# Kernel tuning notes

Hardware: AMD Instinct MI355X
Metric: run time of the kernel (lower is better)

The kernel has to match this reference:

```python
import jax, jax.numpy as jnp
import numpy as np

N = 524288          # events per batch
NUM_NODES = 1_000_000
D = 64              # memory_dim


def gru_cell(x, h, W_ih, W_hh, b_ih, b_hh):
    # torch.nn.GRUCell math; gates ordered (r, z, n)
    gi = x @ W_ih.T + b_ih          # [N, 3D]
    gh = h @ W_hh.T + b_hh          # [N, 3D]
    i_r, i_z, i_n = jnp.split(gi, 3, axis=-1)
    h_r, h_z, h_n = jnp.split(gh, 3, axis=-1)
    r = jax.nn.sigmoid(i_r + h_r)
    z = jax.nn.sigmoid(i_z + h_z)
    n = jnp.tanh(i_n + r * h_n)
    return (1.0 - z) * n + z * h


def setup_inputs() -> dict:
    key = jax.random.key(0)
    ks = jax.random.split(key, 9)
    scale = 1.0 / np.sqrt(D).astype(np.float32)
    return {
        "node_ids": jax.random.randint(ks[0], (N,), 0, NUM_NODES, dtype=jnp.int64)
        if jax.config.jax_enable_x64 else jax.random.randint(ks[0], (N,), 0, NUM_NODES, dtype=jnp.int32),
        "node_embeddings": jax.random.normal(ks[1], (N, D), jnp.float32),
        "timestamps": jax.random.uniform(ks[2], (N,), jnp.float32) * 1000.0,
        "node_memory": jax.random.normal(ks[3], (NUM_NODES, D), jnp.float32) * 0.1,
        "last_update_time": jax.random.uniform(ks[4], (NUM_NODES,), jnp.float32) * 500.0,
        "W_time": jax.random.normal(ks[5], (1, D), jnp.float32) * 0.1,
        "b_time": jnp.zeros((D,), jnp.float32),
        "W_ih": jax.random.normal(ks[6], (3 * D, D), jnp.float32) * scale,
        "W_hh": jax.random.normal(ks[7], (3 * D, D), jnp.float32) * scale,
        "b_ih": jnp.zeros((3 * D,), jnp.float32),
        "b_hh": jnp.zeros((3 * D,), jnp.float32),
    }


def reference(node_ids, node_embeddings, timestamps, node_memory, last_update_time,
              W_time, b_time, W_ih, W_hh, b_ih, b_hh):
    # gather persistent state
    current_memory = node_memory[node_ids]                          # [N, D]
    time_deltas = timestamps - last_update_time[node_ids]           # [N]
    # nn.Linear(1, D): out = dt * W_time[0] + b_time
    time_encoding = time_deltas[:, None] * W_time[0] + b_time       # [N, D]
    updated_memory = gru_cell(node_embeddings + time_encoding, current_memory,
                              W_ih, W_hh, b_ih, b_hh)               # [N, D]
    # scatter write-back (detached in torch)
    new_node_memory = node_memory.at[node_ids].set(jax.lax.stop_gradient(updated_memory))
    new_last_update_time = last_update_time.at[node_ids].set(jax.lax.stop_gradient(timestamps))
    return updated_memory, new_node_memory, new_last_update_time
```

## Files before the change

kernel.cpp:

```cpp
#include <hip/hip_runtime.h>
#include <cstdint>
#include <cstddef>

#define DD 64

typedef float    f32x4  __attribute__((ext_vector_type(4)));
typedef _Float16 f16x8  __attribute__((ext_vector_type(8)));
typedef _Float16 f16x4  __attribute__((ext_vector_type(4)));

__device__ __forceinline__ float sigmoidf_(float x) {
    return 1.0f / (1.0f + __expf(-x));
}
__device__ __forceinline__ float tanh_fast(float x) {
    float ax = fabsf(x);
    float t = 1.0f - 2.0f / (1.0f + __expf(2.0f * ax));
    return copysignf(t, x);
}
__device__ __forceinline__ f32x4 MFMA(f32x4 c, f16x8 a, f16x8 b) {
    return __builtin_amdgcn_mfma_f32_16x16x32_f16(a, b, c, 0, 0, 0);
}

__global__ void k_init(int* __restrict__ winner, int num_nodes) {
    int i = blockIdx.x * blockDim.x + threadIdx.x;
    if (i < num_nodes) winner[i] = -1;
}
__global__ void k_vote(const int* __restrict__ ids, int* __restrict__ winner, int n) {
    int i = blockIdx.x * blockDim.x + threadIdx.x;
    if (i < n) atomicMax(&winner[ids[i]], i);
}

__global__ void k_prep(const float* __restrict__ Wih, const float* __restrict__ Whh,
                       _Float16* __restrict__ bhi, _Float16* __restrict__ blo)
{
    int f = blockIdx.x;
    int l = threadIdx.x;
    int g = f >> 2, s = f & 3;
    int c = g * 16 + (l & 15);
    int grp = c >> 6, d = c & 63;
    int kbase = s * 32 + (l >> 4) * 8;
    int row = (grp == 0) ? d : (grp == 1) ? 64 + d : 128 + d;

    f16x8 hv, lv;
    for (int j = 0; j < 8; ++j) {
        int k = kbase + j;
        float v;
        if (grp <= 1)      v = (k < 64) ? Wih[row * 64 + k] : Whh[row * 64 + (k - 64)];
        else if (grp == 2) v = (k < 64) ? Wih[row * 64 + k] : 0.0f;
        else               v = (k < 64) ? 0.0f : Whh[row * 64 + (k - 64)];
        _Float16 h = (_Float16)v;
        hv[j] = h;
        lv[j] = (_Float16)(v - (float)h);
    }
    size_t off = ((size_t)f * 64 + l);
    ((f16x8*)bhi)[off] = hv;
    ((f16x8*)blo)[off] = lv;
}

__global__ __launch_bounds__(256, 3) void k_gru(
    const int* __restrict__ ids,
    const float* __restrict__ emb,
    const float* __restrict__ ts,
    const float* __restrict__ mem,
    const float* __restrict__ lut,
    const float* __restrict__ Wt,
    const float* __restrict__ bt,
    const float* __restrict__ bih,
    const float* __restrict__ bhh,
    const _Float16* __restrict__ bhi,
    const _Float16* __restrict__ blo,
    const int* __restrict__ winner,
    float* __restrict__ out0,
    float* __restrict__ out1,
    int n)
{
    __shared__ _Float16 xhh[64][136];
    __shared__ _Float16 xhl[64][72];
    __shared__ int sid[64];
    __shared__ int swin[64];

    const int w    = threadIdx.x >> 6;
    const int l    = threadIdx.x & 63;
    const int col  = l & 15;
    const int rowg = l >> 4;
    const int d    = w * 16 + col;

    const long base = (long)blockIdx.x * 64;
    const bool full = (base + 64 <= (long)n);

    const int  e16 = w * 16 + col;
    const long evA = base + e16;
    int idA = 0, winA = 0; float dtA = 0.f;
    if (full || evA < n) {
        idA  = ids[evA];
        dtA  = ts[evA] - lut[idA];
        winA = (winner[idA] == (int)evA) ? 1 : 0;
    }
    if (l < 16) { sid[e16] = idA; swin[e16] = winA; }

    f32x4 xv0, xv1, xv2, xv3, hv0, hv1, hv2, hv3;
    float dt0, dt1, dt2, dt3;
    {
        int   i0 = __shfl(idA, 0 * 4 + rowg), i1 = __shfl(idA, 1 * 4 + rowg);
        int   i2 = __shfl(idA, 2 * 4 + rowg), i3 = __shfl(idA, 3 * 4 + rowg);
        dt0 = __shfl(dtA, 0 * 4 + rowg); dt1 = __shfl(dtA, 1 * 4 + rowg);
        dt2 = __shfl(dtA, 2 * 4 + rowg); dt3 = __shfl(dtA, 3 * 4 + rowg);
        const f32x4* emb4 = (const f32x4*)emb;
        const f32x4* mem4 = (const f32x4*)mem;
        const size_t e0 = (size_t)(base + w * 16 + 0 * 4 + rowg) * 16 + col;
        const size_t e1 = (size_t)(base + w * 16 + 1 * 4 + rowg) * 16 + col;
        const size_t e2 = (size_t)(base + w * 16 + 2 * 4 + rowg) * 16 + col;
        const size_t e3 = (size_t)(base + w * 16 + 3 * 4 + rowg) * 16 + col;
        if (full) {
            xv0 = __builtin_nontemporal_load(&emb4[e0]);
            xv1 = __builtin_nontemporal_load(&emb4[e1]);
            xv2 = __builtin_nontemporal_load(&emb4[e2]);
            xv3 = __builtin_nontemporal_load(&emb4[e3]);
            hv0 = mem4[(size_t)i0 * 16 + col];
            hv1 = mem4[(size_t)i1 * 16 + col];
            hv2 = mem4[(size_t)i2 * 16 + col];
            hv3 = mem4[(size_t)i3 * 16 + col];
        } else {
            f32x4 z = {0.f, 0.f, 0.f, 0.f};
            xv0 = xv1 = xv2 = xv3 = hv0 = hv1 = hv2 = hv3 = z;
            if (base + w * 16 + 0 * 4 + rowg < n) { xv0 = emb4[e0]; hv0 = mem4[(size_t)i0 * 16 + col]; }
            if (base + w * 16 + 1 * 4 + rowg < n) { xv1 = emb4[e1]; hv1 = mem4[(size_t)i1 * 16 + col]; }
            if (base + w * 16 + 2 * 4 + rowg < n) { xv2 = emb4[e2]; hv2 = mem4[(size_t)i2 * 16 + col]; }
            if (base + w * 16 + 3 * 4 + rowg < n) { xv3 = emb4[e3]; hv3 = mem4[(size_t)i3 * 16 + col]; }
        }
    }

    const f32x4 wt4 = ((const f32x4*)Wt)[col];
    const f32x4 bt4 = ((const f32x4*)bt)[col];
    {
        #define CONV_WRITE(XV, HV, DT, IT)                                           \
        {                                                                            \
            int r = w * 16 + (IT) * 4 + rowg;                                        \
            f32x4 x = XV;                                                            \
            x.x = fmaf(DT, wt4.x, x.x + bt4.x);                                      \
            x.y = fmaf(DT, wt4.y, x.y + bt4.y);                                      \
            x.z = fmaf(DT, wt4.z, x.z + bt4.z);                                      \
            x.w = fmaf(DT, wt4.w, x.w + bt4.w);                                      \
            f16x4 xh, xl, hh;                                                        \
            _Float16 a;                                                              \
            a = (_Float16)x.x; xh[0] = a; xl[0] = (_Float16)(x.x - (float)a);        \
            a = (_Float16)x.y; xh[1] = a; xl[1] = (_Float16)(x.y - (float)a);        \
            a = (_Float16)x.z; xh[2] = a; xl[2] = (_Float16)(x.z - (float)a);        \
            a = (_Float16)x.w; xh[3] = a; xl[3] = (_Float16)(x.w - (float)a);        \
            hh[0] = (_Float16)(HV).x; hh[1] = (_Float16)(HV).y;                      \
            hh[2] = (_Float16)(HV).z; hh[3] = (_Float16)(HV).w;                      \
            *(f16x4*)&xhh[r][col * 4]      = xh;                                     \
            *(f16x4*)&xhl[r][col * 4]      = xl;                                     \
            *(f16x4*)&xhh[r][64 + col * 4] = hh;                                     \
        }
        CONV_WRITE(xv0, hv0, dt0, 0)
        CONV_WRITE(xv1, hv1, dt1, 1)
        CONV_WRITE(xv2, hv2, dt2, 2)
        CONV_WRITE(xv3, hv3, dt3, 3)
        #undef CONV_WRITE
    }

    const f16x8* H = (const f16x8*)bhi;
    const f16x8* L = (const f16x8*)blo;
    f16x8 BRh0 = H[(size_t)(w * 4 + 0) * 64 + l];
    f16x8 BRh1 = H[(size_t)(w * 4 + 1) * 64 + l];
    f16x8 BRh2 = H[(size_t)(w * 4 + 2) * 64 + l];
    f16x8 BRh3 = H[(size_t)(w * 4 + 3) * 64 + l];
    f16x8 BRl0 = L[(size_t)(w * 4 + 0) * 64 + l];
    f16x8 BRl1 = L[(size_t)(w * 4 + 1) * 64 + l];
    f16x8 BZh0 = H[(size_t)((4 + w) * 4 + 0) * 64 + l];
    f16x8 BZh1 = H[(size_t)((4 + w) * 4 + 1) * 64 + l];
    f16x8 BZh2 = H[(size_t)((4 + w) * 4 + 2) * 64 + l];
    f16x8 BZh3 = H[(size_t)((4 + w) * 4 + 3) * 64 + l];
    f16x8 BZl0 = L[(size_t)((4 + w) * 4 + 0) * 64 + l];
    f16x8 BZl1 = L[(size_t)((4 + w) * 4 + 1) * 64 + l];
    f16x8 BIh0 = H[(size_t)((8 + w) * 4 + 0) * 64 + l];
    f16x8 BIh1 = H[(size_t)((8 + w) * 4 + 1) * 64 + l];
    f16x8 BIl0 = L[(size_t)((8 + w) * 4 + 0) * 64 + l];
    f16x8 BIl1 = L[(size_t)((8 + w) * 4 + 1) * 64 + l];
    f16x8 BHh0 = H[(size_t)((12 + w) * 4 + 2) * 64 + l];
    f16x8 BHh1 = H[(size_t)((12 + w) * 4 + 3) * 64 + l];

    const float bR  = bih[d] + bhh[d];
    const float bZ  = bih[64 + d] + bhh[64 + d];
    const float bIN = bih[128 + d];
    const float bHN = bhh[128 + d];

    __syncthreads();

    #pragma unroll
    for (int mt = 0; mt < 4; ++mt) {
        const int arow = mt * 16 + col;
        const int k0   = rowg * 8;
        f16x8 Ah0 = *(const f16x8*)&xhh[arow][0 * 32 + k0];
        f16x8 Ah1 = *(const f16x8*)&xhh[arow][1 * 32 + k0];
        f16x8 Ah2 = *(const f16x8*)&xhh[arow][2 * 32 + k0];
        f16x8 Ah3 = *(const f16x8*)&xhh[arow][3 * 32 + k0];
        f16x8 Al0 = *(const f16x8*)&xhl[arow][0 * 32 + k0];
        f16x8 Al1 = *(const f16x8*)&xhl[arow][1 * 32 + k0];

        f32x4 aR = {0,0,0,0}, aZ = {0,0,0,0}, aI = {0,0,0,0}, aH = {0,0,0,0};
        __builtin_amdgcn_s_setprio(1);
        aR = MFMA(aR, Ah0, BRh0); aR = MFMA(aR, Ah0, BRl0); aR = MFMA(aR, Al0, BRh0);
        aR = MFMA(aR, Ah1, BRh1); aR = MFMA(aR, Ah1, BRl1); aR = MFMA(aR, Al1, BRh1);
        aR = MFMA(aR, Ah2, BRh2); aR = MFMA(aR, Ah3, BRh3);
        aZ = MFMA(aZ, Ah0, BZh0); aZ = MFMA(aZ, Ah0, BZl0); aZ = MFMA(aZ, Al0, BZh0);
        aZ = MFMA(aZ, Ah1, BZh1); aZ = MFMA(aZ, Ah1, BZl1); aZ = MFMA(aZ, Al1, BZh1);
        aZ = MFMA(aZ, Ah2, BZh2); aZ = MFMA(aZ, Ah3, BZh3);
        aI = MFMA(aI, Ah0, BIh0); aI = MFMA(aI, Ah0, BIl0); aI = MFMA(aI, Al0, BIh0);
        aI = MFMA(aI, Ah1, BIh1); aI = MFMA(aI, Ah1, BIl1); aI = MFMA(aI, Al1, BIh1);
        aH = MFMA(aH, Ah2, BHh0); aH = MFMA(aH, Ah3, BHh1);
        __builtin_amdgcn_s_setprio(0);

        #pragma unroll
        for (int r = 0; r < 4; ++r) {
            int  eloc = mt * 16 + rowg * 4 + r;
            long ev   = base + eloc;
            if (full || ev < n) {
                float rr = sigmoidf_(aR[r] + bR);
                float zz = sigmoidf_(aZ[r] + bZ);
                float nn = tanh_fast(aI[r] + bIN + rr * (aH[r] + bHN));
                float hv = (float)xhh[eloc][64 + d];
                float o  = (1.f - zz) * nn + zz * hv;
                __builtin_nontemporal_store(o, &out0[(size_t)ev * 64 + d]);
                if (swin[eloc])
                    __builtin_nontemporal_store(o, &out1[(size_t)sid[eloc] * 64 + d]);
            }
        }
    }
}

__global__ void k_tail(float* out2,
                       const f32x4* __restrict__ mem4,
                       f32x4* __restrict__ out14,
                       const float* __restrict__ ts,
                       const float* __restrict__ lut,
                       int num_nodes)
{
    int idx = blockIdx.x * blockDim.x + threadIdx.x;
    if (idx >= num_nodes * 16) return;
    int nidx = idx >> 4;
    int c    = idx & 15;
    int wv = reinterpret_cast<const int*>(out2)[nidx];
    if (wv < 0) {
        f32x4 v = __builtin_nontemporal_load(&mem4[idx]);
        __builtin_nontemporal_store(v, &out14[idx]);
    }
    if (c == 0) out2[nidx] = (wv >= 0) ? ts[wv] : lut[nidx];
}

extern "C" void kernel_launch(void* const* d_in, const int* in_sizes, int n_in,
                              void* d_out, int out_size, void* d_ws, size_t ws_size,
                              hipStream_t stream) {
    const int*   ids = (const int*)  d_in[0];
    const float* emb = (const float*)d_in[1];
    const float* ts  = (const float*)d_in[2];
    const float* mem = (const float*)d_in[3];
    const float* lut = (const float*)d_in[4];
    const float* Wt  = (const float*)d_in[5];
    const float* bt  = (const float*)d_in[6];
    const float* Wih = (const float*)d_in[7];
    const float* Whh = (const float*)d_in[8];
    const float* bih = (const float*)d_in[9];
    const float* bhh = (const float*)d_in[10];

    const int N         = in_sizes[0];
    const int NUM_NODES = in_sizes[4];

    float* out0 = (float*)d_out;
    float* out1 = out0 + (size_t)N * DD;
    float* out2 = out1 + (size_t)NUM_NODES * DD;
    int*   winner = (int*)out2;

    _Float16* bfragH = (_Float16*)d_ws;
    _Float16* bfragL = bfragH + 64 * 64 * 8;

    k_prep<<<64, 64, 0, stream>>>(Wih, Whh, bfragH, bfragL);
    k_init<<<(NUM_NODES + 255) / 256, 256, 0, stream>>>(winner, NUM_NODES);
    k_vote<<<(N + 255) / 256, 256, 0, stream>>>(ids, winner, N);

    int nchunks = (N + 63) / 64;
    k_gru<<<nchunks, 256, 0, stream>>>(ids, emb, ts, mem, lut, Wt, bt, bih, bhh,
                                       bfragH, bfragL, winner, out0, out1, N);

    long vec = (long)NUM_NODES * 16;
    k_tail<<<(int)((vec + 255) / 256), 256, 0, stream>>>(
        out2, (const f32x4*)mem, (f32x4*)out1, ts, lut, NUM_NODES);
}
```

Before: 233.0 us.

## Process two 64-event chunks per GRU block, fuse prep/init, widen tail copy

The GRU kernel now handles 128 events per block. It issues all gathers and embedding loads for both halves up front, so the second half's memory latency overlaps the first half's MFMA and epilogue. Weight fragments are loaded once per 128 events instead of once per 64. The weight-prep and winner-init kernels are merged into one launch, and the tail copy now moves 64 bytes per thread instead of 16. In exchange there is more register pressure from holding 16 f32x4 values, which may hurt occupancy under launch_bounds(256,3). The tail kernel also gets less coalescing per instruction.

```diff
diff --git a/kernel.cpp b/kernel.cpp
--- a/kernel.cpp
+++ b/kernel.cpp
@@ -20,40 +20,42 @@
     return __builtin_amdgcn_mfma_f32_16x16x32_f16(a, b, c, 0, 0, 0);
 }
 
-__global__ void k_init(int* __restrict__ winner, int num_nodes) {
-    int i = blockIdx.x * blockDim.x + threadIdx.x;
-    if (i < num_nodes) winner[i] = -1;
-}
+__global__ void k_prep_init(const float* __restrict__ Wih, const float* __restrict__ Whh,
+                            _Float16* __restrict__ bhi, _Float16* __restrict__ blo,
+                            int* __restrict__ winner, int num_nodes)
+{
+    if (blockIdx.x < 16) {
+        int f = blockIdx.x * 4 + (threadIdx.x >> 6);
+        int l = threadIdx.x & 63;
+        int g = f >> 2, s = f & 3;
+        int c = g * 16 + (l & 15);
+        int grp = c >> 6, dd = c & 63;
+        int kbase = s * 32 + (l >> 4) * 8;
+        int row = (grp == 0) ? dd : (grp == 1) ? 64 + dd : 128 + dd;
+
+        f16x8 hv, lv;
+        for (int j = 0; j < 8; ++j) {
+            int k = kbase + j;
+            float v;
+            if (grp <= 1)      v = (k < 64) ? Wih[row * 64 + k] : Whh[row * 64 + (k - 64)];
+            else if (grp == 2) v = (k < 64) ? Wih[row * 64 + k] : 0.0f;
+            else               v = (k < 64) ? 0.0f : Whh[row * 64 + (k - 64)];
+            _Float16 h = (_Float16)v;
+            hv[j] = h;
+            lv[j] = (_Float16)(v - (float)h);
+        }
+        size_t off = ((size_t)f * 64 + l);
+        ((f16x8*)bhi)[off] = hv;
+        ((f16x8*)blo)[off] = lv;
+    } else {
+        int i = (int)(blockIdx.x - 16) * 256 + threadIdx.x;
+        if (i < num_nodes) winner[i] = -1;
+    }
+}
+
 __global__ void k_vote(const int* __restrict__ ids, int* __restrict__ winner, int n) {
     int i = blockIdx.x * blockDim.x + threadIdx.x;
     if (i < n) atomicMax(&winner[ids[i]], i);
-}
-
-__global__ void k_prep(const float* __restrict__ Wih, const float* __restrict__ Whh,
-                       _Float16* __restrict__ bhi, _Float16* __restrict__ blo)
-{
-    int f = blockIdx.x;
-    int l = threadIdx.x;
-    int g = f >> 2, s = f & 3;
-    int c = g * 16 + (l & 15);
-    int grp = c >> 6, d = c & 63;
-    int kbase = s * 32 + (l >> 4) * 8;
-    int row = (grp == 0) ? d : (grp == 1) ? 64 + d : 128 + d;
-
-    f16x8 hv, lv;
-    for (int j = 0; j < 8; ++j) {
-        int k = kbase + j;
-        float v;
-        if (grp <= 1)      v = (k < 64) ? Wih[row * 64 + k] : Whh[row * 64 + (k - 64)];
-        else if (grp == 2) v = (k < 64) ? Wih[row * 64 + k] : 0.0f;
-        else               v = (k < 64) ? 0.0f : Whh[row * 64 + (k - 64)];
-        _Float16 h = (_Float16)v;
-        hv[j] = h;
-        lv[j] = (_Float16)(v - (float)h);
-    }
-    size_t off = ((size_t)f * 64 + l);
-    ((f16x8*)bhi)[off] = hv;
-    ((f16x8*)blo)[off] = lv;
 }
 
 __global__ __launch_bounds__(256, 3) void k_gru(
@@ -75,89 +77,14 @@
 {
     __shared__ _Float16 xhh[64][136];
     __shared__ _Float16 xhl[64][72];
-    __shared__ int sid[64];
-    __shared__ int swin[64];
+    __shared__ int sid[128];
+    __shared__ int swin[128];
 
     const int w    = threadIdx.x >> 6;
     const int l    = threadIdx.x & 63;
     const int col  = l & 15;
     const int rowg = l >> 4;
     const int d    = w * 16 + col;
-
-    const long base = (long)blockIdx.x * 64;
-    const bool full = (base + 64 <= (long)n);
-
-    const int  e16 = w * 16 + col;
-    const long evA = base + e16;
-    int idA = 0, winA = 0; float dtA = 0.f;
-    if (full || evA < n) {
-        idA  = ids[evA];
-        dtA  = ts[evA] - lut[idA];
-        winA = (winner[idA] == (int)evA) ? 1 : 0;
-    }
-    if (l < 16) { sid[e16] = idA; swin[e16] = winA; }
-
-    f32x4 xv0, xv1, xv2, xv3, hv0, hv1, hv2, hv3;
-    float dt0, dt1, dt2, dt3;
-    {
-        int   i0 = __shfl(idA, 0 * 4 + rowg), i1 = __shfl(idA, 1 * 4 + rowg);
-        int   i2 = __shfl(idA, 2 * 4 + rowg), i3 = __shfl(idA, 3 * 4 + rowg);
-        dt0 = __shfl(dtA, 0 * 4 + rowg); dt1 = __shfl(dtA, 1 * 4 + rowg);
-        dt2 = __shfl(dtA, 2 * 4 + rowg); dt3 = __shfl(dtA, 3 * 4 + rowg);
-        const f32x4* emb4 = (const f32x4*)emb;
-        const f32x4* mem4 = (const f32x4*)mem;
-        const size_t e0 = (size_t)(base + w * 16 + 0 * 4 + rowg) * 16 + col;
-        const size_t e1 = (size_t)(base + w * 16 + 1 * 4 + rowg) * 16 + col;
-        const size_t e2 = (size_t)(base + w * 16 + 2 * 4 + rowg) * 16 + col;
-        const size_t e3 = (size_t)(base + w * 16 + 3 * 4 + rowg) * 16 + col;
-        if (full) {
-            xv0 = __builtin_nontemporal_load(&emb4[e0]);
-            xv1 = __builtin_nontemporal_load(&emb4[e1]);
-            xv2 = __builtin_nontemporal_load(&emb4[e2]);
-            xv3 = __builtin_nontemporal_load(&emb4[e3]);
-            hv0 = mem4[(size_t)i0 * 16 + col];
-            hv1 = mem4[(size_t)i1 * 16 + col];
-            hv2 = mem4[(size_t)i2 * 16 + col];
-            hv3 = mem4[(size_t)i3 * 16 + col];
-        } else {
-            f32x4 z = {0.f, 0.f, 0.f, 0.f};
-            xv0 = xv1 = xv2 = xv3 = hv0 = hv1 = hv2 = hv3 = z;
-            if (base + w * 16 + 0 * 4 + rowg < n) { xv0 = emb4[e0]; hv0 = mem4[(size_t)i0 * 16 + col]; }
-            if (base + w * 16 + 1 * 4 + rowg < n) { xv1 = emb4[e1]; hv1 = mem4[(size_t)i1 * 16 + col]; }
-            if (base + w * 16 + 2 * 4 + rowg < n) { xv2 = emb4[e2]; hv2 = mem4[(size_t)i2 * 16 + col]; }
-            if (base + w * 16 + 3 * 4 + rowg < n) { xv3 = emb4[e3]; hv3 = mem4[(size_t)i3 * 16 + col]; }
-        }
-    }
-
-    const f32x4 wt4 = ((const f32x4*)Wt)[col];
-    const f32x4 bt4 = ((const f32x4*)bt)[col];
-    {
-        #define CONV_WRITE(XV, HV, DT, IT)                                           \
-        {                                                                            \
-            int r = w * 16 + (IT) * 4 + rowg;                                        \
-            f32x4 x = XV;                                                            \
-            x.x = fmaf(DT, wt4.x, x.x + bt4.x);                                      \
-            x.y = fmaf(DT, wt4.y, x.y + bt4.y);                                      \
-            x.z = fmaf(DT, wt4.z, x.z + bt4.z);                                      \
-            x.w = fmaf(DT, wt4.w, x.w + bt4.w);                                      \
-            f16x4 xh, xl, hh;                                                        \
-            _Float16 a;                                                              \
-            a = (_Float16)x.x; xh[0] = a; xl[0] = (_Float16)(x.x - (float)a);        \
-            a = (_Float16)x.y; xh[1] = a; xl[1] = (_Float16)(x.y - (float)a);        \
-            a = (_Float16)x.z; xh[2] = a; xl[2] = (_Float16)(x.z - (float)a);        \
-            a = (_Float16)x.w; xh[3] = a; xl[3] = (_Float16)(x.w - (float)a);        \
-            hh[0] = (_Float16)(HV).x; hh[1] = (_Float16)(HV).y;                      \
-            hh[2] = (_Float16)(HV).z; hh[3] = (_Float16)(HV).w;                      \
-            *(f16x4*)&xhh[r][col * 4]      = xh;                                     \
-            *(f16x4*)&xhl[r][col * 4]      = xl;                                     \
-            *(f16x4*)&xhh[r][64 + col * 4] = hh;                                     \
-        }
-        CONV_WRITE(xv0, hv0, dt0, 0)
-        CONV_WRITE(xv1, hv1, dt1, 1)
-        CONV_WRITE(xv2, hv2, dt2, 2)
-        CONV_WRITE(xv3, hv3, dt3, 3)
-        #undef CONV_WRITE
-    }
 
     const f16x8* H = (const f16x8*)bhi;
     const f16x8* L = (const f16x8*)blo;
@@ -180,53 +107,164 @@
     f16x8 BHh0 = H[(size_t)((12 + w) * 4 + 2) * 64 + l];
     f16x8 BHh1 = H[(size_t)((12 + w) * 4 + 3) * 64 + l];
 
+    const f32x4 wt4 = ((const f32x4*)Wt)[col];
+    const f32x4 bt4 = ((const f32x4*)bt)[col];
     const float bR  = bih[d] + bhh[d];
     const float bZ  = bih[64 + d] + bhh[64 + d];
     const float bIN = bih[128 + d];
     const float bHN = bhh[128 + d];
 
+    const long base = (long)blockIdx.x * 128;
+    const bool full = (base + 128 <= (long)n);
+
+    const int  e16 = w * 16 + col;
+    const long evA = base + e16;
+    const long evB = evA + 64;
+    int idA = 0, winA = 0, idB = 0, winB = 0;
+    float dtA = 0.f, dtB = 0.f;
+    if (full || evA < n) {
+        idA  = ids[evA];
+        dtA  = ts[evA] - lut[idA];
+        winA = (winner[idA] == (int)evA) ? 1 : 0;
+    }
+    if (full || evB < n) {
+        idB  = ids[evB];
+        dtB  = ts[evB] - lut[idB];
+        winB = (winner[idB] == (int)evB) ? 1 : 0;
+    }
+    if (l < 16) {
+        sid[e16]       = idA;  swin[e16]       = winA;
+        sid[64 + e16]  = idB;  swin[64 + e16]  = winB;
+    }
+
+    int ia0 = __shfl(idA, 0 + rowg),  ia1 = __shfl(idA, 4 + rowg);
+    int ia2 = __shfl(idA, 8 + rowg),  ia3 = __shfl(idA, 12 + rowg);
+    int ib0 = __shfl(idB, 0 + rowg),  ib1 = __shfl(idB, 4 + rowg);
+    int ib2 = __shfl(idB, 8 + rowg),  ib3 = __shfl(idB, 12 + rowg);
+    float da0 = __shfl(dtA, 0 + rowg), da1 = __shfl(dtA, 4 + rowg);
+    float da2 = __shfl(dtA, 8 + rowg), da3 = __shfl(dtA, 12 + rowg);
+    float db0 = __shfl(dtB, 0 + rowg), db1 = __shfl(dtB, 4 + rowg);
+    float db2 = __shfl(dtB, 8 + rowg), db3 = __shfl(dtB, 12 + rowg);
+
+    const f32x4* emb4 = (const f32x4*)emb;
+    const f32x4* mem4 = (const f32x4*)mem;
+    f32x4 xa0, xa1, xa2, xa3, ha0, ha1, ha2, ha3;
+    f32x4 xb0, xb1, xb2, xb3, hb0, hb1, hb2, hb3;
+    if (full) {
+        xa0 = __builtin_nontemporal_load(&emb4[(size_t)(base + w * 16 + 0 + rowg) * 16 + col]);
+        xa1 = __builtin_nontemporal_load(&emb4[(size_t)(base + w * 16 + 4 + rowg) * 16 + col]);
+        xa2 = __builtin_nontemporal_load(&emb4[(size_t)(base + w * 16 + 8 + rowg) * 16 + col]);
+        xa3 = __builtin_nontemporal_load(&emb4[(size_t)(base + w * 16 + 12 + rowg) * 16 + col]);
+        xb0 = __builtin_nontemporal_load(&emb4[(size_t)(base + 64 + w * 16 + 0 + rowg) * 16 + col]);
+        xb1 = __builtin_nontemporal_load(&emb4[(size_t)(base + 64 + w * 16 + 4 + rowg) * 16 + col]);
+        xb2 = __builtin_nontemporal_load(&emb4[(size_t)(base + 64 + w * 16 + 8 + rowg) * 16 + col]);
+        xb3 = __builtin_nontemporal_load(&emb4[(size_t)(base + 64 + w * 16 + 12 + rowg) * 16 + col]);
+        ha0 = mem4[(size_t)ia0 * 16 + col];
+        ha1 = mem4[(size_t)ia1 * 16 + col];
+        ha2 = mem4[(size_t)ia2 * 16 + col];
+        ha3 = mem4[(size_t)ia3 * 16 + col];
+        hb0 = mem4[(size_t)ib0 * 16 + col];
+        hb1 = mem4[(size_t)ib1 * 16 + col];
+        hb2 = mem4[(size_t)ib2 * 16 + col];
+        hb3 = mem4[(size_t)ib3 * 16 + col];
+    } else {
+        f32x4 z = {0.f, 0.f, 0.f, 0.f};
+        xa0 = xa1 = xa2 = xa3 = ha0 = ha1 = ha2 = ha3 = z;
+        xb0 = xb1 = xb2 = xb3 = hb0 = hb1 = hb2 = hb3 = z;
+        if (base + w * 16 + 0 + rowg  < n) { xa0 = emb4[(size_t)(base + w * 16 + 0 + rowg) * 16 + col];  ha0 = mem4[(size_t)ia0 * 16 + col]; }
+        if (base + w * 16 + 4 + rowg  < n) { xa1 = emb4[(size_t)(base + w * 16 + 4 + rowg) * 16 + col];  ha1 = mem4[(size_t)ia1 * 16 + col]; }
+        if (base + w * 16 + 8 + rowg  < n) { xa2 = emb4[(size_t)(base + w * 16 + 8 + rowg) * 16 + col];  ha2 = mem4[(size_t)ia2 * 16 + col]; }
+        if (base + w * 16 + 12 + rowg < n) { xa3 = emb4[(size_t)(base + w * 16 + 12 + rowg) * 16 + col]; ha3 = mem4[(size_t)ia3 * 16 + col]; }
+        if (base + 64 + w * 16 + 0 + rowg  < n) { xb0 = emb4[(size_t)(base + 64 + w * 16 + 0 + rowg) * 16 + col];  hb0 = mem4[(size_t)ib0 * 16 + col]; }
+        if (base + 64 + w * 16 + 4 + rowg  < n) { xb1 = emb4[(size_t)(base + 64 + w * 16 + 4 + rowg) * 16 + col];  hb1 = mem4[(size_t)ib1 * 16 + col]; }
+        if (base + 64 + w * 16 + 8 + rowg  < n) { xb2 = emb4[(size_t)(base + 64 + w * 16 + 8 + rowg) * 16 + col];  hb2 = mem4[(size_t)ib2 * 16 + col]; }
+        if (base + 64 + w * 16 + 12 + rowg < n) { xb3 = emb4[(size_t)(base + 64 + w * 16 + 12 + rowg) * 16 + col]; hb3 = mem4[(size_t)ib3 * 16 + col]; }
+    }
+    __builtin_amdgcn_sched_barrier(0);
+
+    #define CONV_WRITE(XV, HV, DT, IT)                                           \
+    {                                                                            \
+        int r = w * 16 + (IT) * 4 + rowg;                                        \
+        f32x4 x = XV;                                                            \
+        x.x = fmaf(DT, wt4.x, x.x + bt4.x);                                      \
+        x.y = fmaf(DT, wt4.y, x.y + bt4.y);                                      \
+        x.z = fmaf(DT, wt4.z, x.z + bt4.z);                                      \
+        x.w = fmaf(DT, wt4.w, x.w + bt4.w);                                      \
+        f16x4 xh, xl, hh;                                                        \
+        _Float16 a;                                                              \
+        a = (_Float16)x.x; xh[0] = a; xl[0] = (_Float16)(x.x - (float)a);        \
+        a = (_Float16)x.y; xh[1] = a; xl[1] = (_Float16)(x.y - (float)a);        \
+        a = (_Float16)x.z; xh[2] = a; xl[2] = (_Float16)(x.z - (float)a);        \
+        a = (_Float16)x.w; xh[3] = a; xl[3] = (_Float16)(x.w - (float)a);        \
+        hh[0] = (_Float16)(HV).x; hh[1] = (_Float16)(HV).y;                      \
+        hh[2] = (_Float16)(HV).z; hh[3] = (_Float16)(HV).w;                      \
+        *(f16x4*)&xhh[r][col * 4]      = xh;                                     \
+        *(f16x4*)&xhl[r][col * 4]      = xl;                                     \
+        *(f16x4*)&xhh[r][64 + col * 4] = hh;                                     \
+    }
+
+    #define DO_MFMA_EPI(CB)                                                      \
+    {                                                                            \
+        _Pragma("unroll")                                                        \
+        for (int mt = 0; mt < 4; ++mt) {                                         \
+            const int arow = mt * 16 + col;                                      \
+            const int k0   = rowg * 8;                                           \
+            f16x8 Ah0 = *(const f16x8*)&xhh[arow][0 * 32 + k0];                  \
+            f16x8 Ah1 = *(const f16x8*)&xhh[arow][1 * 32 + k0];                  \
+            f16x8 Ah2 = *(const f16x8*)&xhh[arow][2 * 32 + k0];                  \
+            f16x8 Ah3 = *(const f16x8*)&xhh[arow][3 * 32 + k0];                  \
+            f16x8 Al0 = *(const f16x8*)&xhl[arow][0 * 32 + k0];                  \
+            f16x8 Al1 = *(const f16x8*)&xhl[arow][1 * 32 + k0];                  \
+            f32x4 aR = {0,0,0,0}, aZ = {0,0,0,0}, aI = {0,0,0,0}, aH = {0,0,0,0};\
+            __builtin_amdgcn_s_setprio(1);                                       \
+            aR = MFMA(aR, Ah0, BRh0); aR = MFMA(aR, Ah0, BRl0);                  \
+            aR = MFMA(aR, Al0, BRh0); aR = MFMA(aR, Ah1, BRh1);                  \
+            aR = MFMA(aR, Ah1, BRl1); aR = MFMA(aR, Al1, BRh1);                  \
+            aR = MFMA(aR, Ah2, BRh2); aR = MFMA(aR, Ah3, BRh3);                  \
+            aZ = MFMA(aZ, Ah0, BZh0); aZ = MFMA(aZ, Ah0, BZl0);                  \
+            aZ = MFMA(aZ, Al0, BZh0); aZ = MFMA(aZ, Ah1, BZh1);                  \
+            aZ = MFMA(aZ, Ah1, BZl1); aZ = MFMA(aZ, Al1, BZh1);                  \
+            aZ = MFMA(aZ, Ah2, BZh2); aZ = MFMA(aZ, Ah3, BZh3);                  \
+            aI = MFMA(aI, Ah0, BIh0); aI = MFMA(aI, Ah0, BIl0);                  \
+            aI = MFMA(aI, Al0, BIh0); aI = MFMA(aI, Ah1, BIh1);                  \
+            aI = MFMA(aI, Ah1, BIl1); aI = MFMA(aI, Al1, BIh1);                  \
+            aH = MFMA(aH, Ah2, BHh0); aH = MFMA(aH, Ah3, BHh1);                  \
+            __builtin_amdgcn_s_setprio(0);                                       \
+            _Pragma("unroll")                                                    \
+            for (int r = 0; r < 4; ++r) {                                        \
+                int  eloc = mt * 16 + rowg * 4 + r;                              \
+                long ev   = base + (CB) + eloc;                                  \
+                if (full || ev < n) {                                            \
+                    float rr = sigmoidf_(aR[r] + bR);                            \
+                    float zz = sigmoidf_(aZ[r] + bZ);                            \
+                    float nn = tanh_fast(aI[r] + bIN + rr * (aH[r] + bHN));      \
+                    float hv = (float)xhh[eloc][64 + d];                         \
+                    float o  = (1.f - zz) * nn + zz * hv;                        \
+                    __builtin_nontemporal_store(o, &out0[(size_t)ev * 64 + d]);  \
+                    if (swin[(CB) + eloc])                                       \
+                        __builtin_nontemporal_store(o, &out1[(size_t)sid[(CB) + eloc] * 64 + d]); \
+                }                                                                \
+            }                                                                    \
+        }                                                                        \
+    }
+
+    CONV_WRITE(xa0, ha0, da0, 0)
+    CONV_WRITE(xa1, ha1, da1, 1)
+    CONV_WRITE(xa2, ha2, da2, 2)
+    CONV_WRITE(xa3, ha3, da3, 3)
     __syncthreads();
-
-    #pragma unroll
-    for (int mt = 0; mt < 4; ++mt) {
-        const int arow = mt * 16 + col;
-        const int k0   = rowg * 8;
-        f16x8 Ah0 = *(const f16x8*)&xhh[arow][0 * 32 + k0];
-        f16x8 Ah1 = *(const f16x8*)&xhh[arow][1 * 32 + k0];
-        f16x8 Ah2 = *(const f16x8*)&xhh[arow][2 * 32 + k0];
-        f16x8 Ah3 = *(const f16x8*)&xhh[arow][3 * 32 + k0];
-        f16x8 Al0 = *(const f16x8*)&xhl[arow][0 * 32 + k0];
-        f16x8 Al1 = *(const f16x8*)&xhl[arow][1 * 32 + k0];
-
-        f32x4 aR = {0,0,0,0}, aZ = {0,0,0,0}, aI = {0,0,0,0}, aH = {0,0,0,0};
-        __builtin_amdgcn_s_setprio(1);
-        aR = MFMA(aR, Ah0, BRh0); aR = MFMA(aR, Ah0, BRl0); aR = MFMA(aR, Al0, BRh0);
-        aR = MFMA(aR, Ah1, BRh1); aR = MFMA(aR, Ah1, BRl1); aR = MFMA(aR, Al1, BRh1);
-        aR = MFMA(aR, Ah2, BRh2); aR = MFMA(aR, Ah3, BRh3);
-        aZ = MFMA(aZ, Ah0, BZh0); aZ = MFMA(aZ, Ah0, BZl0); aZ = MFMA(aZ, Al0, BZh0);
-        aZ = MFMA(aZ, Ah1, BZh1); aZ = MFMA(aZ, Ah1, BZl1); aZ = MFMA(aZ, Al1, BZh1);
-        aZ = MFMA(aZ, Ah2, BZh2); aZ = MFMA(aZ, Ah3, BZh3);
-        aI = MFMA(aI, Ah0, BIh0); aI = MFMA(aI, Ah0, BIl0); aI = MFMA(aI, Al0, BIh0);
-        aI = MFMA(aI, Ah1, BIh1); aI = MFMA(aI, Ah1, BIl1); aI = MFMA(aI, Al1, BIh1);
-        aH = MFMA(aH, Ah2, BHh0); aH = MFMA(aH, Ah3, BHh1);
-        __builtin_amdgcn_s_setprio(0);
-
-        #pragma unroll
-        for (int r = 0; r < 4; ++r) {
-            int  eloc = mt * 16 + rowg * 4 + r;
-            long ev   = base + eloc;
-            if (full || ev < n) {
-                float rr = sigmoidf_(aR[r] + bR);
-                float zz = sigmoidf_(aZ[r] + bZ);
-                float nn = tanh_fast(aI[r] + bIN + rr * (aH[r] + bHN));
-                float hv = (float)xhh[eloc][64 + d];
-                float o  = (1.f - zz) * nn + zz * hv;
-                __builtin_nontemporal_store(o, &out0[(size_t)ev * 64 + d]);
-                if (swin[eloc])
-                    __builtin_nontemporal_store(o, &out1[(size_t)sid[eloc] * 64 + d]);
-            }
-        }
-    }
+    DO_MFMA_EPI(0)
+    __syncthreads();
+
+    CONV_WRITE(xb0, hb0, db0, 0)
+    CONV_WRITE(xb1, hb1, db1, 1)
+    CONV_WRITE(xb2, hb2, db2, 2)
+    CONV_WRITE(xb3, hb3, db3, 3)
+    __syncthreads();
+    DO_MFMA_EPI(64)
+
+    #undef CONV_WRITE
+    #undef DO_MFMA_EPI
 }
 
 __global__ void k_tail(float* out2,
@@ -236,16 +274,23 @@
                        const float* __restrict__ lut,
                        int num_nodes)
 {
-    int idx = blockIdx.x * blockDim.x + threadIdx.x;
-    if (idx >= num_nodes * 16) return;
-    int nidx = idx >> 4;
-    int c    = idx & 15;
-    int wv = reinterpret_cast<const int*>(out2)[nidx];
+    int idx  = blockIdx.x * blockDim.x + threadIdx.x;
+    int node = idx >> 2;
+    int q    = idx & 3;
+    if (node >= num_nodes) return;
+    int wv = reinterpret_cast<const int*>(out2)[node];
     if (wv < 0) {
-        f32x4 v = __builtin_nontemporal_load(&mem4[idx]);
-        __builtin_nontemporal_store(v, &out14[idx]);
-    }
-    if (c == 0) out2[nidx] = (wv >= 0) ? ts[wv] : lut[nidx];
+        size_t o = (size_t)node * 16 + q * 4;
+        f32x4 v0 = __builtin_nontemporal_load(&mem4[o + 0]);
+        f32x4 v1 = __builtin_nontemporal_load(&mem4[o + 1]);
+        f32x4 v2 = __builtin_nontemporal_load(&mem4[o + 2]);
+        f32x4 v3 = __builtin_nontemporal_load(&mem4[o + 3]);
+        __builtin_nontemporal_store(v0, &out14[o + 0]);
+        __builtin_nontemporal_store(v1, &out14[o + 1]);
+        __builtin_nontemporal_store(v2, &out14[o + 2]);
+        __builtin_nontemporal_store(v3, &out14[o + 3]);
+    }
+    if (q == 0) out2[node] = (wv >= 0) ? ts[wv] : lut[node];
 }
 
 extern "C" void kernel_launch(void* const* d_in, const int* in_sizes, int n_in,
@@ -274,15 +319,16 @@
     _Float16* bfragH = (_Float16*)d_ws;
     _Float16* bfragL = bfragH + 64 * 64 * 8;
 
-    k_prep<<<64, 64, 0, stream>>>(Wih, Whh, bfragH, bfragL);
-    k_init<<<(NUM_NODES + 255) / 256, 256, 0, stream>>>(winner, NUM_NODES);
+    int initBlocks = (NUM_NODES + 255) / 256;
+    k_prep_init<<<16 + initBlocks, 256, 0, stream>>>(Wih, Whh, bfragH, bfragL,
+                                                     winner, NUM_NODES);
     k_vote<<<(N + 255) / 256, 256, 0, stream>>>(ids, winner, N);
 
-    int nchunks = (N + 63) / 64;
-    k_gru<<<nchunks, 256, 0, stream>>>(ids, emb, ts, mem, lut, Wt, bt, bih, bhh,
-                                       bfragH, bfragL, winner, out0, out1, N);
-
-    long vec = (long)NUM_NODES * 16;
-    k_tail<<<(int)((vec + 255) / 256), 256, 0, stream>>>(
+    int gruBlocks = (N + 127) / 128;
+    k_gru<<<gruBlocks, 256, 0, stream>>>(ids, emb, ts, mem, lut, Wt, bt, bih, bhh,
+                                         bfragH, bfragL, winner, out0, out1, N);
+
+    long tailThreads = (long)NUM_NODES * 4;
+    k_tail<<<(int)((tailThreads + 255) / 256), 256, 0, stream>>>(
         out2, (const f32x4*)mem, (f32x4*)out1, ts, lut, NUM_NODES);
 }
```

New measurement: 423.5 us. +81.7%, slower.

## Stage GRU inputs via direct global-to-LDS loads, merge prep/init, widen tail copies

Applied to the files above, without the earlier changes.

The embedding and gathered memory rows are now loaded with global_load_lds straight into a shared-memory union, then read back, converted to split fp16 and rewritten in place over the same buffer. The goal is to cut register pressure and give better load overlap. The weight prep and winner-init kernels are merged into one launch to save a launch. The tail copy kernel now has each thread move four 16-byte vectors instead of one. The cost is extra __syncthreads, a round trip through LDS, and fewer threads in the tail kernel.

```diff
diff --git a/kernel.cpp b/kernel.cpp
--- a/kernel.cpp
+++ b/kernel.cpp
@@ -19,41 +19,49 @@
 __device__ __forceinline__ f32x4 MFMA(f32x4 c, f16x8 a, f16x8 b) {
     return __builtin_amdgcn_mfma_f32_16x16x32_f16(a, b, c, 0, 0, 0);
 }
-
-__global__ void k_init(int* __restrict__ winner, int num_nodes) {
-    int i = blockIdx.x * blockDim.x + threadIdx.x;
-    if (i < num_nodes) winner[i] = -1;
-}
+__device__ __forceinline__ void gl2lds16(const void* g, void* l) {
+    __builtin_amdgcn_global_load_lds(
+        (const __attribute__((address_space(1))) void*)g,
+        (__attribute__((address_space(3))) void*)l,
+        16, 0, 0);
+}
+
+__global__ void k_prep_init(const float* __restrict__ Wih, const float* __restrict__ Whh,
+                            _Float16* __restrict__ bhi, _Float16* __restrict__ blo,
+                            int* __restrict__ winner, int num_nodes)
+{
+    if (blockIdx.x < 16) {
+        int f = blockIdx.x * 4 + (threadIdx.x >> 6);
+        int l = threadIdx.x & 63;
+        int g = f >> 2, s = f & 3;
+        int c = g * 16 + (l & 15);
+        int grp = c >> 6, dd = c & 63;
+        int kbase = s * 32 + (l >> 4) * 8;
+        int row = (grp == 0) ? dd : (grp == 1) ? 64 + dd : 128 + dd;
+
+        f16x8 hv, lv;
+        for (int j = 0; j < 8; ++j) {
+            int k = kbase + j;
+            float v;
+            if (grp <= 1)      v = (k < 64) ? Wih[row * 64 + k] : Whh[row * 64 + (k - 64)];
+            else if (grp == 2) v = (k < 64) ? Wih[row * 64 + k] : 0.0f;
+            else               v = (k < 64) ? 0.0f : Whh[row * 64 + (k - 64)];
+            _Float16 h = (_Float16)v;
+            hv[j] = h;
+            lv[j] = (_Float16)(v - (float)h);
+        }
+        size_t off = ((size_t)f * 64 + l);
+        ((f16x8*)bhi)[off] = hv;
+        ((f16x8*)blo)[off] = lv;
+    } else {
+        int i = (int)(blockIdx.x - 16) * 256 + threadIdx.x;
+        if (i < num_nodes) winner[i] = -1;
+    }
+}
+
 __global__ void k_vote(const int* __restrict__ ids, int* __restrict__ winner, int n) {
     int i = blockIdx.x * blockDim.x + threadIdx.x;
     if (i < n) atomicMax(&winner[ids[i]], i);
-}
-
-__global__ void k_prep(const float* __restrict__ Wih, const float* __restrict__ Whh,
-                       _Float16* __restrict__ bhi, _Float16* __restrict__ blo)
-{
-    int f = blockIdx.x;
-    int l = threadIdx.x;
-    int g = f >> 2, s = f & 3;
-    int c = g * 16 + (l & 15);
-    int grp = c >> 6, d = c & 63;
-    int kbase = s * 32 + (l >> 4) * 8;
-    int row = (grp == 0) ? d : (grp == 1) ? 64 + d : 128 + d;
-
-    f16x8 hv, lv;
-    for (int j = 0; j < 8; ++j) {
-        int k = kbase + j;
-        float v;
-        if (grp <= 1)      v = (k < 64) ? Wih[row * 64 + k] : Whh[row * 64 + (k - 64)];
-        else if (grp == 2) v = (k < 64) ? Wih[row * 64 + k] : 0.0f;
-        else               v = (k < 64) ? 0.0f : Whh[row * 64 + (k - 64)];
-        _Float16 h = (_Float16)v;
-        hv[j] = h;
-        lv[j] = (_Float16)(v - (float)h);
-    }
-    size_t off = ((size_t)f * 64 + l);
-    ((f16x8*)bhi)[off] = hv;
-    ((f16x8*)blo)[off] = lv;
 }
 
 __global__ __launch_bounds__(256, 3) void k_gru(
@@ -73,8 +81,10 @@
     float* __restrict__ out1,
     int n)
 {
-    __shared__ _Float16 xhh[64][136];
-    __shared__ _Float16 xhl[64][72];
+    __shared__ __align__(16) union {
+        struct { float x[64][64]; float h[64][64]; } raw;
+        struct { _Float16 hh[64][136]; _Float16 hl[64][72]; } fr;
+    } u;
     __shared__ int sid[64];
     __shared__ int swin[64];
 
@@ -86,6 +96,13 @@
 
     const long base = (long)blockIdx.x * 64;
     const bool full = (base + 64 <= (long)n);
+
+    if (full) {
+        gl2lds16(emb + (size_t)(base + w * 16 + 0  + rowg) * 64 + col * 4, &u.raw.x[w * 16 + 0][0]);
+        gl2lds16(emb + (size_t)(base + w * 16 + 4  + rowg) * 64 + col * 4, &u.raw.x[w * 16 + 4][0]);
+        gl2lds16(emb + (size_t)(base + w * 16 + 8  + rowg) * 64 + col * 4, &u.raw.x[w * 16 + 8][0]);
+        gl2lds16(emb + (size_t)(base + w * 16 + 12 + rowg) * 64 + col * 4, &u.raw.x[w * 16 + 12][0]);
+    }
 
     const int  e16 = w * 16 + col;
     const long evA = base + e16;
@@ -95,69 +112,35 @@
         dtA  = ts[evA] - lut[idA];
         winA = (winner[idA] == (int)evA) ? 1 : 0;
     }
+
+    int ia0 = __shfl(idA, 0 + rowg),  ia1 = __shfl(idA, 4 + rowg);
+    int ia2 = __shfl(idA, 8 + rowg),  ia3 = __shfl(idA, 12 + rowg);
+    float da0 = __shfl(dtA, 0 + rowg), da1 = __shfl(dtA, 4 + rowg);
+    float da2 = __shfl(dtA, 8 + rowg), da3 = __shfl(dtA, 12 + rowg);
+
+    if (full) {
+        gl2lds16(mem + (size_t)ia0 * 64 + col * 4, &u.raw.h[w * 16 + 0][0]);
+        gl2lds16(mem + (size_t)ia1 * 64 + col * 4, &u.raw.h[w * 16 + 4][0]);
+        gl2lds16(mem + (size_t)ia2 * 64 + col * 4, &u.raw.h[w * 16 + 8][0]);
+        gl2lds16(mem + (size_t)ia3 * 64 + col * 4, &u.raw.h[w * 16 + 12][0]);
+    } else {
+        #pragma unroll
+        for (int it = 0; it < 4; ++it) {
+            int  r  = w * 16 + it * 4 + rowg;
+            long ev = base + r;
+            int idt = __shfl(idA, it * 4 + rowg);
+            f32x4 xv = {0.f, 0.f, 0.f, 0.f};
+            f32x4 hv = {0.f, 0.f, 0.f, 0.f};
+            if (ev < n) {
+                xv = ((const f32x4*)emb)[(size_t)ev * 16 + col];
+                hv = ((const f32x4*)mem)[(size_t)idt * 16 + col];
+            }
+            *(f32x4*)&u.raw.x[r][col * 4] = xv;
+            *(f32x4*)&u.raw.h[r][col * 4] = hv;
+        }
+    }
+
     if (l < 16) { sid[e16] = idA; swin[e16] = winA; }
-
-    f32x4 xv0, xv1, xv2, xv3, hv0, hv1, hv2, hv3;
-    float dt0, dt1, dt2, dt3;
-    {
-        int   i0 = __shfl(idA, 0 * 4 + rowg), i1 = __shfl(idA, 1 * 4 + rowg);
-        int   i2 = __shfl(idA, 2 * 4 + rowg), i3 = __shfl(idA, 3 * 4 + rowg);
-        dt0 = __shfl(dtA, 0 * 4 + rowg); dt1 = __shfl(dtA, 1 * 4 + rowg);
-        dt2 = __shfl(dtA, 2 * 4 + rowg); dt3 = __shfl(dtA, 3 * 4 + rowg);
-        const f32x4* emb4 = (const f32x4*)emb;
-        const f32x4* mem4 = (const f32x4*)mem;
-        const size_t e0 = (size_t)(base + w * 16 + 0 * 4 + rowg) * 16 + col;
-        const size_t e1 = (size_t)(base + w * 16 + 1 * 4 + rowg) * 16 + col;
-        const size_t e2 = (size_t)(base + w * 16 + 2 * 4 + rowg) * 16 + col;
-        const size_t e3 = (size_t)(base + w * 16 + 3 * 4 + rowg) * 16 + col;
-        if (full) {
-            xv0 = __builtin_nontemporal_load(&emb4[e0]);
-            xv1 = __builtin_nontemporal_load(&emb4[e1]);
-            xv2 = __builtin_nontemporal_load(&emb4[e2]);
-            xv3 = __builtin_nontemporal_load(&emb4[e3]);
-            hv0 = mem4[(size_t)i0 * 16 + col];
-            hv1 = mem4[(size_t)i1 * 16 + col];
-            hv2 = mem4[(size_t)i2 * 16 + col];
-            hv3 = mem4[(size_t)i3 * 16 + col];
-        } else {
-            f32x4 z = {0.f, 0.f, 0.f, 0.f};
-            xv0 = xv1 = xv2 = xv3 = hv0 = hv1 = hv2 = hv3 = z;
-            if (base + w * 16 + 0 * 4 + rowg < n) { xv0 = emb4[e0]; hv0 = mem4[(size_t)i0 * 16 + col]; }
-            if (base + w * 16 + 1 * 4 + rowg < n) { xv1 = emb4[e1]; hv1 = mem4[(size_t)i1 * 16 + col]; }
-            if (base + w * 16 + 2 * 4 + rowg < n) { xv2 = emb4[e2]; hv2 = mem4[(size_t)i2 * 16 + col]; }
-            if (base + w * 16 + 3 * 4 + rowg < n) { xv3 = emb4[e3]; hv3 = mem4[(size_t)i3 * 16 + col]; }
-        }
-    }
-
-    const f32x4 wt4 = ((const f32x4*)Wt)[col];
-    const f32x4 bt4 = ((const f32x4*)bt)[col];
-    {
-        #define CONV_WRITE(XV, HV, DT, IT)                                           \
-        {                                                                            \
-            int r = w * 16 + (IT) * 4 + rowg;                                        \
-            f32x4 x = XV;                                                            \
-            x.x = fmaf(DT, wt4.x, x.x + bt4.x);                                      \
-            x.y = fmaf(DT, wt4.y, x.y + bt4.y);                                      \
-            x.z = fmaf(DT, wt4.z, x.z + bt4.z);                                      \
-            x.w = fmaf(DT, wt4.w, x.w + bt4.w);                                      \
-            f16x4 xh, xl, hh;                                                        \
-            _Float16 a;                                                              \
-            a = (_Float16)x.x; xh[0] = a; xl[0] = (_Float16)(x.x - (float)a);        \
-            a = (_Float16)x.y; xh[1] = a; xl[1] = (_Float16)(x.y - (float)a);        \
-            a = (_Float16)x.z; xh[2] = a; xl[2] = (_Float16)(x.z - (float)a);        \
-            a = (_Float16)x.w; xh[3] = a; xl[3] = (_Float16)(x.w - (float)a);        \
-            hh[0] = (_Float16)(HV).x; hh[1] = (_Float16)(HV).y;                      \
-            hh[2] = (_Float16)(HV).z; hh[3] = (_Float16)(HV).w;                      \
-            *(f16x4*)&xhh[r][col * 4]      = xh;                                     \
-            *(f16x4*)&xhl[r][col * 4]      = xl;                                     \
-            *(f16x4*)&xhh[r][64 + col * 4] = hh;                                     \
-        }
-        CONV_WRITE(xv0, hv0, dt0, 0)
-        CONV_WRITE(xv1, hv1, dt1, 1)
-        CONV_WRITE(xv2, hv2, dt2, 2)
-        CONV_WRITE(xv3, hv3, dt3, 3)
-        #undef CONV_WRITE
-    }
 
     const f16x8* H = (const f16x8*)bhi;
     const f16x8* L = (const f16x8*)blo;
@@ -180,6 +163,8 @@
     f16x8 BHh0 = H[(size_t)((12 + w) * 4 + 2) * 64 + l];
     f16x8 BHh1 = H[(size_t)((12 + w) * 4 + 3) * 64 + l];
 
+    const f32x4 wt4 = ((const f32x4*)Wt)[col];
+    const f32x4 bt4 = ((const f32x4*)bt)[col];
     const float bR  = bih[d] + bhh[d];
     const float bZ  = bih[64 + d] + bhh[64 + d];
     const float bIN = bih[128 + d];
@@ -187,16 +172,55 @@
 
     __syncthreads();
 
+    f32x4 x0 = *(const f32x4*)&u.raw.x[w * 16 + 0  + rowg][col * 4];
+    f32x4 x1 = *(const f32x4*)&u.raw.x[w * 16 + 4  + rowg][col * 4];
+    f32x4 x2 = *(const f32x4*)&u.raw.x[w * 16 + 8  + rowg][col * 4];
+    f32x4 x3 = *(const f32x4*)&u.raw.x[w * 16 + 12 + rowg][col * 4];
+    f32x4 h0 = *(const f32x4*)&u.raw.h[w * 16 + 0  + rowg][col * 4];
+    f32x4 h1 = *(const f32x4*)&u.raw.h[w * 16 + 4  + rowg][col * 4];
+    f32x4 h2 = *(const f32x4*)&u.raw.h[w * 16 + 8  + rowg][col * 4];
+    f32x4 h3 = *(const f32x4*)&u.raw.h[w * 16 + 12 + rowg][col * 4];
+
+    __syncthreads();
+
+    #define CONV_WRITE(XV, HV, DT, IT)                                           \
+    {                                                                            \
+        int r = w * 16 + (IT) * 4 + rowg;                                        \
+        f32x4 x = XV;                                                            \
+        x.x = fmaf(DT, wt4.x, x.x + bt4.x);                                      \
+        x.y = fmaf(DT, wt4.y, x.y + bt4.y);                                      \
+        x.z = fmaf(DT, wt4.z, x.z + bt4.z);                                      \
+        x.w = fmaf(DT, wt4.w, x.w + bt4.w);                                      \
+        f16x4 xh, xl, hh;                                                        \
+        _Float16 a;                                                              \
+        a = (_Float16)x.x; xh[0] = a; xl[0] = (_Float16)(x.x - (float)a);        \
+        a = (_Float16)x.y; xh[1] = a; xl[1] = (_Float16)(x.y - (float)a);        \
+        a = (_Float16)x.z; xh[2] = a; xl[2] = (_Float16)(x.z - (float)a);        \
+        a = (_Float16)x.w; xh[3] = a; xl[3] = (_Float16)(x.w - (float)a);        \
+        hh[0] = (_Float16)(HV).x; hh[1] = (_Float16)(HV).y;                      \
+        hh[2] = (_Float16)(HV).z; hh[3] = (_Float16)(HV).w;                      \
+        *(f16x4*)&u.fr.hh[r][col * 4]      = xh;                                 \
+        *(f16x4*)&u.fr.hl[r][col * 4]      = xl;                                 \
+        *(f16x4*)&u.fr.hh[r][64 + col * 4] = hh;                                 \
+    }
+    CONV_WRITE(x0, h0, da0, 0)
+    CONV_WRITE(x1, h1, da1, 1)
+    CONV_WRITE(x2, h2, da2, 2)
+    CONV_WRITE(x3, h3, da3, 3)
+    #undef CONV_WRITE
+
+    __syncthreads();
+
     #pragma unroll
     for (int mt = 0; mt < 4; ++mt) {
         const int arow = mt * 16 + col;
         const int k0   = rowg * 8;
-        f16x8 Ah0 = *(const f16x8*)&xhh[arow][0 * 32 + k0];
-        f16x8 Ah1 = *(const f16x8*)&xhh[arow][1 * 32 + k0];
-        f16x8 Ah2 = *(const f16x8*)&xhh[arow][2 * 32 + k0];
-        f16x8 Ah3 = *(const f16x8*)&xhh[arow][3 * 32 + k0];
-        f16x8 Al0 = *(const f16x8*)&xhl[arow][0 * 32 + k0];
-        f16x8 Al1 = *(const f16x8*)&xhl[arow][1 * 32 + k0];
+        f16x8 Ah0 = *(const f16x8*)&u.fr.hh[arow][0 * 32 + k0];
+        f16x8 Ah1 = *(const f16x8*)&u.fr.hh[arow][1 * 32 + k0];
+        f16x8 Ah2 = *(const f16x8*)&u.fr.hh[arow][2 * 32 + k0];
+        f16x8 Ah3 = *(const f16x8*)&u.fr.hh[arow][3 * 32 + k0];
+        f16x8 Al0 = *(const f16x8*)&u.fr.hl[arow][0 * 32 + k0];
+        f16x8 Al1 = *(const f16x8*)&u.fr.hl[arow][1 * 32 + k0];
 
         f32x4 aR = {0,0,0,0}, aZ = {0,0,0,0}, aI = {0,0,0,0}, aH = {0,0,0,0};
         __builtin_amdgcn_s_setprio(1);
@@ -219,7 +243,7 @@
                 float rr = sigmoidf_(aR[r] + bR);
                 float zz = sigmoidf_(aZ[r] + bZ);
                 float nn = tanh_fast(aI[r] + bIN + rr * (aH[r] + bHN));
-                float hv = (float)xhh[eloc][64 + d];
+                float hv = (float)u.fr.hh[eloc][64 + d];
                 float o  = (1.f - zz) * nn + zz * hv;
                 __builtin_nontemporal_store(o, &out0[(size_t)ev * 64 + d]);
                 if (swin[eloc])
@@ -236,16 +260,23 @@
                        const float* __restrict__ lut,
                        int num_nodes)
 {
-    int idx = blockIdx.x * blockDim.x + threadIdx.x;
-    if (idx >= num_nodes * 16) return;
-    int nidx = idx >> 4;
-    int c    = idx & 15;
-    int wv = reinterpret_cast<const int*>(out2)[nidx];
+    int idx  = blockIdx.x * blockDim.x + threadIdx.x;
+    int node = idx >> 2;
+    int q    = idx & 3;
+    if (node >= num_nodes) return;
+    int wv = reinterpret_cast<const int*>(out2)[node];
     if (wv < 0) {
-        f32x4 v = __builtin_nontemporal_load(&mem4[idx]);
-        __builtin_nontemporal_store(v, &out14[idx]);
-    }
-    if (c == 0) out2[nidx] = (wv >= 0) ? ts[wv] : lut[nidx];
+        size_t o = (size_t)node * 16 + q * 4;
+        f32x4 v0 = __builtin_nontemporal_load(&mem4[o + 0]);
+        f32x4 v1 = __builtin_nontemporal_load(&mem4[o + 1]);
+        f32x4 v2 = __builtin_nontemporal_load(&mem4[o + 2]);
+        f32x4 v3 = __builtin_nontemporal_load(&mem4[o + 3]);
+        __builtin_nontemporal_store(v0, &out14[o + 0]);
+        __builtin_nontemporal_store(v1, &out14[o + 1]);
+        __builtin_nontemporal_store(v2, &out14[o + 2]);
+        __builtin_nontemporal_store(v3, &out14[o + 3]);
+    }
+    if (q == 0) out2[node] = (wv >= 0) ? ts[wv] : lut[node];
 }
 
 extern "C" void kernel_launch(void* const* d_in, const int* in_sizes, int n_in,
@@ -274,15 +305,16 @@
     _Float16* bfragH = (_Float16*)d_ws;
     _Float16* bfragL = bfragH + 64 * 64 * 8;
 
-    k_prep<<<64, 64, 0, stream>>>(Wih, Whh, bfragH, bfragL);
-    k_init<<<(NUM_NODES + 255) / 256, 256, 0, stream>>>(winner, NUM_NODES);
+    int initBlocks = (NUM_NODES + 255) / 256;
+    k_prep_init<<<16 + initBlocks, 256, 0, stream>>>(Wih, Whh, bfragH, bfragL,
+                                                     winner, NUM_NODES);
     k_vote<<<(N + 255) / 256, 256, 0, stream>>>(ids, winner, N);
 
-    int nchunks = (N + 63) / 64;
-    k_gru<<<nchunks, 256, 0, stream>>>(ids, emb, ts, mem, lut, Wt, bt, bih, bhh,
-                                       bfragH, bfragL, winner, out0, out1, N);
-
-    long vec = (long)NUM_NODES * 16;
-    k_tail<<<(int)((vec + 255) / 256), 256, 0, stream>>>(
+    int gruBlocks = (N + 63) / 64;
+    k_gru<<<gruBlocks, 256, 0, stream>>>(ids, emb, ts, mem, lut, Wt, bt, bih, bhh,
+                                         bfragH, bfragL, winner, out0, out1, N);
+
+    long tailThreads = (long)NUM_NODES * 4;
+    k_tail<<<(int)((tailThreads + 255) / 256), 256, 0, stream>>>(
         out2, (const f32x4*)mem, (f32x4*)out1, ts, lut, NUM_NODES);
 }
```

After: 375.8 us. +61.3%, slower.
